# Optimization experiments

Measured on AMD Instinct MI355X. Metric: run time of the kernel, lower is better.

The kernel has to match this reference:

```python
import jax, jax.numpy as jnp
import numpy as np

B, S, D, R, H = 4, 2048, 1024, 256, 8
NI, NP, NO, K = 8, 32, 8, 3
DH = R // H


def _householder_chain(x, vs):
    # x: [B,S,R], vs: [B,S,K,R]; apply K Householder reflections sequentially
    def step(carry, v):
        vn = v * jax.lax.rsqrt(jnp.sum(v * v, axis=-1, keepdims=True) + 1e-8)
        vTx = jnp.sum(carry * vn, axis=-1, keepdims=True)
        return carry - 2.0 * vn * vTx, None
    out, _ = jax.lax.scan(step, x, jnp.moveaxis(vs, 2, 0))
    return out


def _circuit_down(x, in_neurons, proc_neurons, input_weights, proc_idx):
    # soft mixture of input-neuron projections: d_model -> rank
    all_proj = jnp.einsum('bsd,ndr->bsnr', x, in_neurons)
    xr = jnp.einsum('bsnr,bsn->bsr', all_proj, input_weights)
    return _householder_chain(xr, proc_neurons[proc_idx])


def setup_inputs():
    key = jax.random.key(0)
    ks = jax.random.split(key, 14)
    n = lambda k, shape, sc: jax.random.normal(k, shape, jnp.float32) * sc
    inv_d, inv_r = 1.0 / np.sqrt(D), 1.0 / np.sqrt(R)
    return {
        'x': n(ks[0], (B, S, D), 1.0),
        'q_in': n(ks[1], (NI, D, R), inv_d),
        'q_proc': n(ks[2], (NP, R), inv_r),
        'k_in': n(ks[3], (NI, D, R), inv_d),
        'k_proc': n(ks[4], (NP, R), inv_r),
        'v_in': n(ks[5], (NI, D, R), inv_d),
        'v_proc': n(ks[6], (NP, R), inv_r),
        'o_proc': n(ks[7], (NP, R), inv_r),
        'o_out': n(ks[8], (NO, R, D), inv_r),
        'rd_in': n(ks[9], (NI, D), inv_d),
        'rd_proc': n(ks[10], (NP, D), inv_d),
        'ru_out': n(ks[11], (NO, R), inv_r),
        'ru_proc': n(ks[12], (NP, R), inv_r),
    }


def reference(x, q_in, q_proc, k_in, k_proc, v_in, v_proc, o_proc, o_out,
              rd_in, rd_proc, ru_out, ru_proc):
    # --- router (down): soft input weights + top-k process indices ---
    input_weights = jax.nn.softmax(x @ rd_in.T, axis=-1)          # [B,S,NI]
    _, pidx = jax.lax.top_k(x @ rd_proc.T, K)                     # [B,S,K]

    q = _circuit_down(x, q_in, q_proc, input_weights, pidx)      # [B,S,R]
    k = _circuit_down(x, k_in, k_proc, input_weights, pidx)
    v = _circuit_down(x, v_in, v_proc, input_weights, pidx)

    qh = q.reshape(B, S, H, DH)
    kh = k.reshape(B, S, H, DH)
    vh = v.reshape(B, S, H, DH)
    scores = jnp.einsum('bqhd,bkhd->bhqk', qh, kh) / np.sqrt(DH)
    attn = jax.nn.softmax(scores, axis=-1)
    o = jnp.einsum('bhqk,bkhd->bqhd', attn, vh).reshape(B, S, R)  # [B,S,R]

    # --- router (up): soft output weights + top-k process indices ---
    output_weights = jax.nn.softmax(o @ ru_out.T, axis=-1)        # [B,S,NO]
    _, pidx_u = jax.lax.top_k(o @ ru_proc.T, K)                   # [B,S,K]

    oh = _householder_chain(o, o_proc[pidx_u])                    # [B,S,R]
    out = jnp.einsum('bsr,bsn,nrd->bsd', oh, output_weights, o_out)
    return out
```

## Files before the change

kernel.cpp:

```cpp
#include <hip/hip_runtime.h>
#include <math.h>

#define NI 8
#define NP 32
#define TOPK 3

typedef _Float16 f16;
typedef f16 f16x8 __attribute__((ext_vector_type(8)));
typedef f16 f16x4 __attribute__((ext_vector_type(4)));
typedef float f32x4 __attribute__((ext_vector_type(4)));

__device__ __forceinline__ float wave_sum(float v) {
  #pragma unroll
  for (int off = 32; off; off >>= 1) v += __shfl_xor(v, off);
  return v;
}

__device__ __forceinline__ void gload16(const void* g, void* l) {
  __builtin_amdgcn_global_load_lds(
      (const __attribute__((address_space(1))) unsigned int*)g,
      (__attribute__((address_space(3))) unsigned int*)l, 16, 0, 0);
}

__device__ __forceinline__ void split4(float4 v, f16x4& h, f16x4& l) {
  h[0] = (f16)v.x; l[0] = (f16)(v.x - (float)h[0]);
  h[1] = (f16)v.y; l[1] = (f16)(v.y - (float)h[1]);
  h[2] = (f16)v.z; l[2] = (f16)(v.z - (float)h[2]);
  h[3] = (f16)v.w; l[3] = (f16)(v.w - (float)h[3]);
}

template<int CHUNKS>
__global__ __launch_bounds__(256) void router_v2(
    const float* __restrict__ X,
    const float* __restrict__ Wsm,
    const float* __restrict__ Wtk,
    float* __restrict__ iw, int* __restrict__ pidx,
    f16* __restrict__ Xh, f16* __restrict__ Xl)
{
  const int Kin = CHUNKS * 256;
  const int tid = threadIdx.x, wave = tid >> 6, lane = tid & 63;
  __shared__ float sc[4][4][40];
  const size_t t0 = (size_t)blockIdx.x * 16 + wave * 4;

  float4 xv[4][CHUNKS];
  #pragma unroll
  for (int tt = 0; tt < 4; ++tt) {
    const float4* Xp = reinterpret_cast<const float4*>(X + (t0 + tt) * Kin);
    #pragma unroll
    for (int c = 0; c < CHUNKS; ++c) xv[tt][c] = Xp[c * 64 + lane];
  }
  if (Xh) {
    #pragma unroll
    for (int tt = 0; tt < 4; ++tt)
      #pragma unroll
      for (int c = 0; c < CHUNKS; ++c) {
        f16x4 h, l;
        split4(xv[tt][c], h, l);
        size_t off = (t0 + tt) * Kin + (c * 64 + lane) * 4;
        *reinterpret_cast<f16x4*>(Xh + off) = h;
        *reinterpret_cast<f16x4*>(Xl + off) = l;
      }
  }

  for (int w = 0; w < 40; ++w) {
    const float* Wr = (w < NI) ? (Wsm + (size_t)w * Kin) : (Wtk + (size_t)(w - NI) * Kin);
    const float4* Wp = reinterpret_cast<const float4*>(Wr);
    float p[4] = {};
    #pragma unroll
    for (int c = 0; c < CHUNKS; ++c) {
      float4 wv = Wp[c * 64 + lane];
      #pragma unroll
      for (int tt = 0; tt < 4; ++tt) {
        p[tt] = fmaf(xv[tt][c].x, wv.x, p[tt]);
        p[tt] = fmaf(xv[tt][c].y, wv.y, p[tt]);
        p[tt] = fmaf(xv[tt][c].z, wv.z, p[tt]);
        p[tt] = fmaf(xv[tt][c].w, wv.w, p[tt]);
      }
    }
    #pragma unroll
    for (int tt = 0; tt < 4; ++tt) {
      p[tt] = wave_sum(p[tt]);
      if (lane == 0) sc[wave][tt][w] = p[tt];
    }
  }

  for (int tt = 0; tt < 4; ++tt) {
    float s = (lane < NI) ? sc[wave][tt][lane] : -3.0e38f;
    float m = s;
    #pragma unroll
    for (int off = 4; off; off >>= 1) m = fmaxf(m, __shfl_xor(m, off));
    float e = expf(s - m);
    float sum = e;
    #pragma unroll
    for (int off = 4; off; off >>= 1) sum += __shfl_xor(sum, off);
    if (lane < NI) iw[(t0 + tt) * NI + lane] = e / sum;

    float v = (lane < NP) ? sc[wave][tt][NI + lane] : -3.0e38f;
    int idx = lane;
    #pragma unroll
    for (int j = 0; j < TOPK; ++j) {
      float bv = v; int bi = idx;
      #pragma unroll
      for (int off = 32; off; off >>= 1) {
        float ov = __shfl_xor(bv, off); int oi = __shfl_xor(bi, off);
        if (ov > bv || (ov == bv && oi < bi)) { bv = ov; bi = oi; }
      }
      if (lane == 0) pidx[(t0 + tt) * TOPK + j] = bi;
      if (idx == bi) v = -3.0e38f;
    }
  }
}

__global__ __launch_bounds__(256) void pack_bt(
    const float* __restrict__ S, f16* __restrict__ Dh, f16* __restrict__ Dl,
    int C, int K)
{
  __shared__ float T[64][65];
  const int tid = threadIdx.x;
  const int kb = blockIdx.x * 64, cb = blockIdx.y * 64;
  const int tr = tid >> 4, tc = (tid & 15) * 4;
  #pragma unroll
  for (int i = 0; i < 4; ++i) {
    float4 v = *reinterpret_cast<const float4*>(&S[(size_t)(kb + tr + i * 16) * C + cb + tc]);
    T[tr + i * 16][tc + 0] = v.x; T[tr + i * 16][tc + 1] = v.y;
    T[tr + i * 16][tc + 2] = v.z; T[tr + i * 16][tc + 3] = v.w;
  }
  __syncthreads();
  #pragma unroll
  for (int i = 0; i < 4; ++i) {
    int c = tr + i * 16;
    f16x4 vh, vl;
    #pragma unroll
    for (int q = 0; q < 4; ++q) {
      float a = T[tc + q][c];
      f16 h = (f16)a;
      vh[q] = h;
      vl[q] = (f16)(a - (float)h);
    }
    *reinterpret_cast<f16x4*>(&Dh[(size_t)(cb + c) * K + kb + tc]) = vh;
    *reinterpret_cast<f16x4*>(&Dl[(size_t)(cb + c) * K + kb + tc]) = vl;
  }
}

#define TBM 128
#define TBK 32

template<int NFRAG>
__global__ __launch_bounds__(256, 3) void gemm_split2(
    const f16* __restrict__ Xh, const f16* __restrict__ Xl, int Kin,
    const float* __restrict__ W,
    const f16* __restrict__ Bth, const f16* __restrict__ Btl,
    float* __restrict__ C, int ldC, int Ktot)
{
  const int TBN = 32 * NFRAG;
  __shared__ f16x8 AhL[512];
  __shared__ f16x8 AlL[512];
  __shared__ f16x8 BhL[TBN * 4];
  __shared__ f16x8 BlL[TBN * 4];
  __shared__ float Ws[TBM][NI];

  const int tid = threadIdx.x;
  const int wave = tid >> 6, lane = tid & 63;
  const int wm = wave >> 1, wn = wave & 1;
  const int fr = lane & 15, ks = lane >> 4;
  const int row0 = blockIdx.x * TBM, c0 = blockIdx.y * TBN;

  for (int i = tid; i < TBM * NI; i += 256)
    Ws[i >> 3][i & 7] = W[(size_t)(row0 + (i >> 3)) * NI + (i & 7)];

  const int s1 = 256 + tid;
  const int ar0 = tid >> 2, kg0 = ((tid & 3) - (ar0 >> 1)) & 3;
  const int ar1 = s1 >> 2,  kg1 = ((s1 & 3) - (ar1 >> 1)) & 3;

  const f16* xh0 = Xh + (size_t)(row0 + ar0) * Kin + kg0 * 8;
  const f16* xh1 = Xh + (size_t)(row0 + ar1) * Kin + kg1 * 8;
  const f16* xl0 = Xl + (size_t)(row0 + ar0) * Kin + kg0 * 8;
  const f16* xl1 = Xl + (size_t)(row0 + ar1) * Kin + kg1 * 8;
  const f16* bh0 = Bth + (size_t)(c0 + ar0) * Ktot + kg0 * 8;
  const f16* bl0 = Btl + (size_t)(c0 + ar0) * Ktot + kg0 * 8;
  const int ar1b = (ar1 < TBN) ? ar1 : 0;
  const f16* bh1 = Bth + (size_t)(c0 + ar1b) * Ktot + kg1 * 8;
  const f16* bl1 = Btl + (size_t)(c0 + ar1b) * Ktot + kg1 * 8;
  const bool b2 = (NFRAG == 4) || (wave < 2);

  f16x8* AhW = &AhL[wave * 64];
  f16x8* AlW = &AlL[wave * 64];
  f16x8* BhW = &BhL[wave * 64];
  f16x8* BlW = &BlL[wave * 64];

  f32x4 acc[4][NFRAG] = {};
  f32x4 cac[4][NFRAG] = {};

  int n = 0, dk0 = 0;
  for (int kt = 0; kt < Ktot; kt += TBK) {
    __syncthreads();
    gload16(xh0 + dk0, AhW);
    gload16(xh1 + dk0, AhW + 256);
    gload16(xl0 + dk0, AlW);
    gload16(xl1 + dk0, AlW + 256);
    gload16(bh0 + kt, BhW);
    gload16(bl0 + kt, BlW);
    if (b2) {
      gload16(bh1 + kt, BhW + 256);
      gload16(bl1 + kt, BlW + 256);
    }
    __syncthreads();

    f16x8 ah[4], al[4], bh[NFRAG], bl[NFRAG];
    #pragma unroll
    for (int mf = 0; mf < 4; ++mf) {
      int ar = wm * 64 + mf * 16 + fr;
      int sl = ar * 4 + (((ar >> 1) + ks) & 3);
      ah[mf] = AhL[sl]; al[mf] = AlL[sl];
    }
    #pragma unroll
    for (int nf = 0; nf < NFRAG; ++nf) {
      int bc = wn * (16 * NFRAG) + nf * 16 + fr;
      int sl = bc * 4 + (((bc >> 1) + ks) & 3);
      bh[nf] = BhL[sl]; bl[nf] = BlL[sl];
    }
    #pragma unroll
    for (int mf = 0; mf < 4; ++mf)
      #pragma unroll
      for (int nf = 0; nf < NFRAG; ++nf) {
        acc[mf][nf] = __builtin_amdgcn_mfma_f32_16x16x32_f16(ah[mf], bh[nf], acc[mf][nf], 0, 0, 0);
        acc[mf][nf] = __builtin_amdgcn_mfma_f32_16x16x32_f16(ah[mf], bl[nf], acc[mf][nf], 0, 0, 0);
        acc[mf][nf] = __builtin_amdgcn_mfma_f32_16x16x32_f16(al[mf], bh[nf], acc[mf][nf], 0, 0, 0);
      }

    dk0 += TBK;
    if (dk0 == Kin) {
      dk0 = 0;
      #pragma unroll
      for (int mf = 0; mf < 4; ++mf) {
        float w0 = Ws[wm * 64 + mf * 16 + ks * 4 + 0][n];
        float w1 = Ws[wm * 64 + mf * 16 + ks * 4 + 1][n];
        float w2 = Ws[wm * 64 + mf * 16 + ks * 4 + 2][n];
        float w3 = Ws[wm * 64 + mf * 16 + ks * 4 + 3][n];
        #pragma unroll
        for (int nf = 0; nf < NFRAG; ++nf) {
          cac[mf][nf][0] = fmaf(w0, acc[mf][nf][0], cac[mf][nf][0]);
          cac[mf][nf][1] = fmaf(w1, acc[mf][nf][1], cac[mf][nf][1]);
          cac[mf][nf][2] = fmaf(w2, acc[mf][nf][2], cac[mf][nf][2]);
          cac[mf][nf][3] = fmaf(w3, acc[mf][nf][3], cac[mf][nf][3]);
          acc[mf][nf] = (f32x4){0.f, 0.f, 0.f, 0.f};
        }
      }
      ++n;
    }
  }

  #pragma unroll
  for (int mf = 0; mf < 4; ++mf)
    #pragma unroll
    for (int nf = 0; nf < NFRAG; ++nf) {
      int col = c0 + wn * (16 * NFRAG) + nf * 16 + fr;
      #pragma unroll
      for (int j = 0; j < 4; ++j) {
        int row = row0 + wm * 64 + mf * 16 + ks * 4 + j;
        C[(size_t)row * ldC + col] = cac[mf][nf][j];
      }
    }
}

#define GBM 128
#define GBN 128
#define GBK 16
#define GBMp 132

__global__ __launch_bounds__(256) void gemm_mix(
    const float* __restrict__ X, int Kin,
    const float* __restrict__ W,
    const float* __restrict__ Bm0, const float* __restrict__ Bm1, const float* __restrict__ Bm2,
    int ldB, float* __restrict__ C, int ldC, int Nz)
{
  __shared__ float As[GBK][GBMp];
  __shared__ float Bs[GBK][GBMp];
  __shared__ float Ws[GBM][NI];
  const int tid = threadIdx.x;
  const int row0 = blockIdx.x * GBM;
  const int z = blockIdx.z;
  const float* Bm = (z == 0) ? Bm0 : (z == 1) ? Bm1 : Bm2;
  const int c0 = blockIdx.y * GBN;
  for (int i = tid; i < GBM * NI; i += 256)
    Ws[i >> 3][i & 7] = W[(size_t)(row0 + (i >> 3)) * NI + (i & 7)];
  __syncthreads();

  float acc[8][8] = {};
  const int tr = tid >> 4, tc = tid & 15;
  const int srow = tid >> 2;
  const int sseg = (tid & 3) * 4;
  const int bk = tid >> 4;
  const int bc = (tid & 15) * 4;

  const int Ktot = Kin * NI;
  int n = 0, dk0 = 0;
  for (int kt = 0; kt < Ktot; kt += GBK) {
    __syncthreads();
    #pragma unroll
    for (int p = 0; p < 2; ++p) {
      int r = p * 64 + srow;
      float4 xv = *reinterpret_cast<const float4*>(&X[(size_t)(row0 + r) * Kin + dk0 + sseg]);
      float wgt = Ws[r][n];
      As[sseg + 0][r] = xv.x * wgt;
      As[sseg + 1][r] = xv.y * wgt;
      As[sseg + 2][r] = xv.z * wgt;
      As[sseg + 3][r] = xv.w * wgt;
    }
    #pragma unroll
    for (int p = 0; p < 2; ++p) {
      int cc = p * 64 + bc;
      float4 bv = *reinterpret_cast<const float4*>(&Bm[(size_t)(kt + bk) * ldB + c0 + cc]);
      *reinterpret_cast<float4*>(&Bs[bk][cc]) = bv;
    }
    __syncthreads();
    #pragma unroll
    for (int k = 0; k < GBK; ++k) {
      float4 a0 = *reinterpret_cast<const float4*>(&As[k][tr * 8]);
      float4 a1 = *reinterpret_cast<const float4*>(&As[k][tr * 8 + 4]);
      float4 b0 = *reinterpret_cast<const float4*>(&Bs[k][tc * 8]);
      float4 b1 = *reinterpret_cast<const float4*>(&Bs[k][tc * 8 + 4]);
      float av[8] = {a0.x, a0.y, a0.z, a0.w, a1.x, a1.y, a1.z, a1.w};
      float bv[8] = {b0.x, b0.y, b0.z, b0.w, b1.x, b1.y, b1.z, b1.w};
      #pragma unroll
      for (int i = 0; i < 8; ++i)
        #pragma unroll
        for (int j = 0; j < 8; ++j)
          acc[i][j] = fmaf(av[i], bv[j], acc[i][j]);
    }
    dk0 += GBK;
    if (dk0 == Kin) { dk0 = 0; ++n; }
  }
  #pragma unroll
  for (int i = 0; i < 8; ++i) {
    int row = row0 + tr * 8 + i;
    float* Cp = C + (size_t)row * ldC + z * Nz + c0 + tc * 8;
    float4 o0 = {acc[i][0], acc[i][1], acc[i][2], acc[i][3]};
    float4 o1 = {acc[i][4], acc[i][5], acc[i][6], acc[i][7]};
    *reinterpret_cast<float4*>(Cp) = o0;
    *reinterpret_cast<float4*>(Cp + 4) = o1;
  }
}

__global__ __launch_bounds__(256) void hh_kernel(
    float* __restrict__ X, int ldX,
    const float* __restrict__ P0, const float* __restrict__ P1, const float* __restrict__ P2,
    const int* __restrict__ pidx,
    f16* __restrict__ D0h, f16* __restrict__ D0l,
    f16* __restrict__ D1h, f16* __restrict__ D1l,
    f16* __restrict__ D2h, f16* __restrict__ D2l)
{
  const int tid = threadIdx.x, wave = tid >> 6, lane = tid & 63;
  const int t = blockIdx.x * 4 + wave;
  const int circ = blockIdx.y;
  const float* P = (circ == 0) ? P0 : (circ == 1) ? P1 : P2;
  float* xp = X + (size_t)t * ldX + circ * 256;
  float4 x4 = *reinterpret_cast<float4*>(xp + lane * 4);
  #pragma unroll
  for (int j = 0; j < TOPK; ++j) {
    int id = pidx[t * TOPK + j];
    const float* vp = P + (size_t)id * 256;
    float4 v4 = *reinterpret_cast<const float4*>(vp + lane * 4);
    float ss = v4.x * v4.x + v4.y * v4.y + v4.z * v4.z + v4.w * v4.w;
    ss = wave_sum(ss);
    float inv = 1.0f / sqrtf(ss + 1e-8f);
    float4 vn = {v4.x * inv, v4.y * inv, v4.z * inv, v4.w * inv};
    float dt = vn.x * x4.x + vn.y * x4.y + vn.z * x4.z + vn.w * x4.w;
    dt = wave_sum(dt);
    float d2 = 2.0f * dt;
    x4.x = fmaf(-d2, vn.x, x4.x);
    x4.y = fmaf(-d2, vn.y, x4.y);
    x4.z = fmaf(-d2, vn.z, x4.z);
    x4.w = fmaf(-d2, vn.w, x4.w);
  }
  f16* Dh = (circ == 0) ? D0h : (circ == 1) ? D1h : D2h;
  f16* Dl = (circ == 0) ? D0l : (circ == 1) ? D1l : D2l;
  if (Dh) {
    f16x4 h, l;
    split4(x4, h, l);
    *reinterpret_cast<f16x4*>(Dh + (size_t)t * 256 + lane * 4) = h;
    *reinterpret_cast<f16x4*>(Dl + (size_t)t * 256 + lane * 4) = l;
  } else {
    *reinterpret_cast<float4*>(xp + lane * 4) = x4;
  }
}

__global__ __launch_bounds__(256, 2) void attn_mfma2(
    const float* __restrict__ qkv,
    const f16* __restrict__ Khg, const f16* __restrict__ Klg,
    const f16* __restrict__ Vhg, const f16* __restrict__ Vlg,
    float* __restrict__ O)
{
  __shared__ f16 Kh[64][40], Kl[64][40];
  __shared__ f16 Vh[32][72], Vl[32][72];
  __shared__ f16 Ph[4][32][72], Pl[4][32][72];

  const int tid = threadIdx.x, wave = tid >> 6, lane = tid & 63;
  const int c = lane & 15, g = lane >> 4;
  const int bh = blockIdx.y, b = bh >> 3, h = bh & 7;
  const int q0 = blockIdx.x * 128;
  const size_t tbase = (size_t)b * 2048;
  const float SCALE = 0.17677669529663687f;

  f16x8 qh[2], ql[2];
  #pragma unroll
  for (int qt = 0; qt < 2; ++qt) {
    const int row = q0 + wave * 32 + qt * 16 + c;
    const float* qp = qkv + (tbase + row) * 768 + h * 32 + g * 8;
    float4 a = *reinterpret_cast<const float4*>(qp);
    float4 b4 = *reinterpret_cast<const float4*>(qp + 4);
    float qv[8] = {a.x, a.y, a.z, a.w, b4.x, b4.y, b4.z, b4.w};
    #pragma unroll
    for (int j = 0; j < 8; ++j) {
      float xs = qv[j] * SCALE;
      f16 hh = (f16)xs;
      qh[qt][j] = hh;
      ql[qt][j] = (f16)(xs - (float)hh);
    }
  }

  f32x4 sacc[2][4];
  f32x4 oacc[2][2] = {};
  float mrow[2][4] = {{-INFINITY, -INFINITY, -INFINITY, -INFINITY},
                      {-INFINITY, -INFINITY, -INFINITY, -INFINITY}};
  float lrow[2][4] = {};

  for (int k0 = 0; k0 < 2048; k0 += 64) {
    __syncthreads();
    {
      const int kj = tid >> 2, dq = (tid & 3) * 8;
      const size_t krow = (tbase + k0 + kj) * 256 + h * 32 + dq;
      *reinterpret_cast<f16x8*>(&Kh[kj][dq]) = *reinterpret_cast<const f16x8*>(Khg + krow);
      *reinterpret_cast<f16x8*>(&Kl[kj][dq]) = *reinterpret_cast<const f16x8*>(Klg + krow);

      const int vk = tid & 63, vq = (tid >> 6) * 8;
      const size_t vrow = (tbase + k0 + vk) * 256 + h * 32 + vq;
      f16x8 vh8 = *reinterpret_cast<const f16x8*>(Vhg + vrow);
      f16x8 vl8 = *reinterpret_cast<const f16x8*>(Vlg + vrow);
      #pragma unroll
      for (int j = 0; j < 8; ++j) { Vh[vq + j][vk] = vh8[j]; Vl[vq + j][vk] = vl8[j]; }
    }
    __syncthreads();

    #pragma unroll
    for (int s = 0; s < 4; ++s) {
      f16x8 kbh = *reinterpret_cast<const f16x8*>(&Kh[s * 16 + c][g * 8]);
      f16x8 kbl = *reinterpret_cast<const f16x8*>(&Kl[s * 16 + c][g * 8]);
      #pragma unroll
      for (int qt = 0; qt < 2; ++qt) {
        f32x4 acc = {0.f, 0.f, 0.f, 0.f};
        acc = __builtin_amdgcn_mfma_f32_16x16x32_f16(qh[qt], kbh, acc, 0, 0, 0);
        acc = __builtin_amdgcn_mfma_f32_16x16x32_f16(qh[qt], kbl, acc, 0, 0, 0);
        acc = __builtin_amdgcn_mfma_f32_16x16x32_f16(ql[qt], kbh, acc, 0, 0, 0);
        sacc[qt][s] = acc;
      }
    }

    float alpha[2][4];
    #pragma unroll
    for (int qt = 0; qt < 2; ++qt)
      #pragma unroll
      for (int r = 0; r < 4; ++r) {
        float mt = fmaxf(fmaxf(sacc[qt][0][r], sacc[qt][1][r]),
                         fmaxf(sacc[qt][2][r], sacc[qt][3][r]));
        #pragma unroll
        for (int off = 1; off < 16; off <<= 1) mt = fmaxf(mt, __shfl_xor(mt, off));
        float mn = fmaxf(mrow[qt][r], mt);
        float al = __expf(mrow[qt][r] - mn);
        mrow[qt][r] = mn;
        alpha[qt][r] = al;
        float ps = 0.f;
        #pragma unroll
        for (int s = 0; s < 4; ++s) {
          float p = __expf(sacc[qt][s][r] - mn);
          sacc[qt][s][r] = p;
          ps += p;
        }
        #pragma unroll
        for (int off = 1; off < 16; off <<= 1) ps += __shfl_xor(ps, off);
        lrow[qt][r] = lrow[qt][r] * al + ps;
      }

    #pragma unroll
    for (int qt = 0; qt < 2; ++qt)
      #pragma unroll
      for (int s = 0; s < 4; ++s)
        #pragma unroll
        for (int r = 0; r < 4; ++r) {
          float p = sacc[qt][s][r];
          f16 hh = (f16)p;
          Ph[wave][qt * 16 + g * 4 + r][s * 16 + c] = hh;
          Pl[wave][qt * 16 + g * 4 + r][s * 16 + c] = (f16)(p - (float)hh);
        }

    #pragma unroll
    for (int qt = 0; qt < 2; ++qt)
      #pragma unroll
      for (int dh = 0; dh < 2; ++dh)
        #pragma unroll
        for (int r = 0; r < 4; ++r) oacc[qt][dh][r] *= alpha[qt][r];

    #pragma unroll
    for (int ch = 0; ch < 2; ++ch) {
      f16x8 pah[2], pal[2];
      #pragma unroll
      for (int qt = 0; qt < 2; ++qt) {
        pah[qt] = *reinterpret_cast<const f16x8*>(&Ph[wave][qt * 16 + c][ch * 32 + g * 8]);
        pal[qt] = *reinterpret_cast<const f16x8*>(&Pl[wave][qt * 16 + c][ch * 32 + g * 8]);
      }
      #pragma unroll
      for (int dh = 0; dh < 2; ++dh) {
        f16x8 vh = *reinterpret_cast<const f16x8*>(&Vh[dh * 16 + c][ch * 32 + g * 8]);
        f16x8 vl = *reinterpret_cast<const f16x8*>(&Vl[dh * 16 + c][ch * 32 + g * 8]);
        #pragma unroll
        for (int qt = 0; qt < 2; ++qt) {
          oacc[qt][dh] = __builtin_amdgcn_mfma_f32_16x16x32_f16(pah[qt], vh, oacc[qt][dh], 0, 0, 0);
          oacc[qt][dh] = __builtin_amdgcn_mfma_f32_16x16x32_f16(pah[qt], vl, oacc[qt][dh], 0, 0, 0);
          oacc[qt][dh] = __builtin_amdgcn_mfma_f32_16x16x32_f16(pal[qt], vh, oacc[qt][dh], 0, 0, 0);
        }
      }
    }
  }

  #pragma unroll
  for (int qt = 0; qt < 2; ++qt)
    #pragma unroll
    for (int r = 0; r < 4; ++r) {
      float inv = 1.0f / lrow[qt][r];
      int row = q0 + wave * 32 + qt * 16 + g * 4 + r;
      #pragma unroll
      for (int dh = 0; dh < 2; ++dh)
        O[(tbase + row) * 256 + h * 32 + dh * 16 + c] = oacc[qt][dh][r] * inv;
    }
}

__global__ __launch_bounds__(256) void attn_kernel(
    const float* __restrict__ qkv, float* __restrict__ O)
{
  const int tid = threadIdx.x;
  const int wave = tid >> 6, lane = tid & 63;
  const int bh = blockIdx.y, b = bh >> 3, h = bh & 7;
  const int q0 = blockIdx.x * 8;
  const size_t tbase = (size_t)b * 2048;
  const float SCALE = 0.17677669529663687f;

  __shared__ float Ks[64][36];
  __shared__ float Vt[32][68];
  __shared__ float Ps[4][2][64];

  const int wq = __builtin_amdgcn_readfirstlane(wave);
  const float* qr0 = qkv + (tbase + q0 + wq * 2) * 768 + h * 32;
  float qa[32], qb[32];
  #pragma unroll
  for (int i = 0; i < 32; ++i) { qa[i] = qr0[i]; qb[i] = qr0[768 + i]; }

  const int r = lane >> 5, d = lane & 31;
  float m0 = -INFINITY, m1 = -INFINITY, l0 = 0.f, l1 = 0.f, oacc = 0.f;

  for (int k0 = 0; k0 < 2048; k0 += 64) {
    __syncthreads();
    {
      int j = tid >> 2;
      int c = (tid & 3) * 8;
      const float* kp = qkv + (tbase + k0 + j) * 768 + 256 + h * 32 + c;
      float4 ka = *reinterpret_cast<const float4*>(kp);
      float4 kb = *reinterpret_cast<const float4*>(kp + 4);
      *reinterpret_cast<float4*>(&Ks[j][c]) = ka;
      *reinterpret_cast<float4*>(&Ks[j][c + 4]) = kb;
      const float* vp = qkv + (tbase + k0 + j) * 768 + 512 + h * 32 + c;
      float4 va = *reinterpret_cast<const float4*>(vp);
      float4 vb = *reinterpret_cast<const float4*>(vp + 4);
      Vt[c + 0][j] = va.x; Vt[c + 1][j] = va.y; Vt[c + 2][j] = va.z; Vt[c + 3][j] = va.w;
      Vt[c + 4][j] = vb.x; Vt[c + 5][j] = vb.y; Vt[c + 6][j] = vb.z; Vt[c + 7][j] = vb.w;
    }
    __syncthreads();
    float s0 = 0.f, s1 = 0.f;
    #pragma unroll
    for (int dd = 0; dd < 8; ++dd) {
      float4 kv = *reinterpret_cast<const float4*>(&Ks[lane][dd * 4]);
      s0 = fmaf(qa[dd * 4 + 0], kv.x, s0); s1 = fmaf(qb[dd * 4 + 0], kv.x, s1);
      s0 = fmaf(qa[dd * 4 + 1], kv.y, s0); s1 = fmaf(qb[dd * 4 + 1], kv.y, s1);
      s0 = fmaf(qa[dd * 4 + 2], kv.z, s0); s1 = fmaf(qb[dd * 4 + 2], kv.z, s1);
      s0 = fmaf(qa[dd * 4 + 3], kv.w, s0); s1 = fmaf(qb[dd * 4 + 3], kv.w, s1);
    }
    s0 *= SCALE; s1 *= SCALE;
    float mx0 = s0, mx1 = s1;
    #pragma unroll
    for (int off = 32; off; off >>= 1) {
      mx0 = fmaxf(mx0, __shfl_xor(mx0, off));
      mx1 = fmaxf(mx1, __shfl_xor(mx1, off));
    }
    float nm0 = fmaxf(m0, mx0), nm1 = fmaxf(m1, mx1);
    float p0 = expf(s0 - nm0), p1 = expf(s1 - nm1);
    float a0 = expf(m0 - nm0), a1 = expf(m1 - nm1);
    float sp0 = p0, sp1 = p1;
    #pragma unroll
    for (int off = 32; off; off >>= 1) {
      sp0 += __shfl_xor(sp0, off);
      sp1 += __shfl_xor(sp1, off);
    }
    l0 = l0 * a0 + sp0; l1 = l1 * a1 + sp1;
    m0 = nm0; m1 = nm1;
    Ps[wave][0][lane] = p0; Ps[wave][1][lane] = p1;
    oacc *= (r == 0) ? a0 : a1;
    #pragma unroll
    for (int jq = 0; jq < 16; ++jq) {
      float4 pv = *reinterpret_cast<const float4*>(&Ps[wave][r][jq * 4]);
      float4 vv = *reinterpret_cast<const float4*>(&Vt[d][jq * 4]);
      oacc = fmaf(pv.x, vv.x, oacc);
      oacc = fmaf(pv.y, vv.y, oacc);
      oacc = fmaf(pv.z, vv.z, oacc);
      oacc = fmaf(pv.w, vv.w, oacc);
    }
  }
  float lf = (r == 0) ? l0 : l1;
  oacc /= lf;
  O[(tbase + q0 + wave * 2 + r) * 256 + h * 32 + d] = oacc;
}

extern "C" void kernel_launch(void* const* d_in, const int* in_sizes, int n_in,
                              void* d_out, int out_size, void* d_ws, size_t ws_size,
                              hipStream_t stream) {
  const float* x       = (const float*)d_in[0];
  const float* q_in    = (const float*)d_in[1];
  const float* q_proc  = (const float*)d_in[2];
  const float* k_in    = (const float*)d_in[3];
  const float* k_proc  = (const float*)d_in[4];
  const float* v_in    = (const float*)d_in[5];
  const float* v_proc  = (const float*)d_in[6];
  const float* o_proc  = (const float*)d_in[7];
  const float* o_out   = (const float*)d_in[8];
  const float* rd_in   = (const float*)d_in[9];
  const float* rd_proc = (const float*)d_in[10];
  const float* ru_out  = (const float*)d_in[11];
  const float* ru_proc = (const float*)d_in[12];
  float* out = (float*)d_out;
  float* qkv = (float*)d_out;

  const size_t NEED2 = (768ull << 10) + 768ull * 8192 * 2 * 2 + 8192ull * 1024 * 2 * 2;

  if (ws_size >= NEED2) {
    char* wsb = (char*)d_ws;
    float* iw    = (float*)wsb;
    float* owt   = (float*)(wsb + (256 << 10));
    int*   pidx  = (int*)(wsb + (512 << 10));
    int*   pidxu = (int*)(wsb + (640 << 10));
    char*  R1    = wsb + (768 << 10);
    f16* bth_q = (f16*)R1;
    f16* btl_q = (f16*)(R1 + 768ull * 8192 * 2);
    char*  R2    = R1 + 768ull * 8192 * 2 * 2;
    f16* Xh = (f16*)R2;
    f16* Xl = (f16*)(R2 + 8192ull * 1024 * 2);
    float* obuf  = (float*)R2;
    f16* Oh    = (f16*)(R2 + 8388608);
    f16* Ol    = (f16*)(R2 + 12582912);
    f16* bth_o = (f16*)(R2 + 16777216);
    f16* btl_o = (f16*)(R2 + 20971520);
    f16* Khg   = (f16*)(R2 + 25165824);
    f16* Klg   = (f16*)(R2 + 29360128);
    f16* Vhg = (f16*)((char*)d_out + 25165824);
    f16* Vlg = (f16*)((char*)d_out + 29360128);

    router_v2<4><<<dim3(512), dim3(256), 0, stream>>>(x, rd_in, rd_proc, iw, pidx, Xh, Xl);
    pack_bt<<<dim3(128, 4), dim3(256), 0, stream>>>(q_in, bth_q,                 btl_q,                 256, 8192);
    pack_bt<<<dim3(128, 4), dim3(256), 0, stream>>>(k_in, bth_q + 256ull * 8192, btl_q + 256ull * 8192, 256, 8192);
    pack_bt<<<dim3(128, 4), dim3(256), 0, stream>>>(v_in, bth_q + 512ull * 8192, btl_q + 512ull * 8192, 256, 8192);
    gemm_split2<3><<<dim3(64, 8), dim3(256), 0, stream>>>(Xh, Xl, 1024, iw, bth_q, btl_q,
                                                          qkv, 768, 8192);
    hh_kernel<<<dim3(2048, 3), dim3(256), 0, stream>>>(qkv, 768, q_proc, k_proc, v_proc, pidx,
                                                       (f16*)nullptr, (f16*)nullptr,
                                                       Khg, Klg, Vhg, Vlg);
    pack_bt<<<dim3(32, 16), dim3(256), 0, stream>>>(o_out, bth_o, btl_o, 1024, 2048);
    attn_mfma2<<<dim3(16, 32), dim3(256), 0, stream>>>(qkv, Khg, Klg, Vhg, Vlg, obuf);
    router_v2<1><<<dim3(512), dim3(256), 0, stream>>>(obuf, ru_out, ru_proc, owt, pidxu,
                                                      (f16*)nullptr, (f16*)nullptr);
    hh_kernel<<<dim3(2048, 1), dim3(256), 0, stream>>>(obuf, 256, o_proc, o_proc, o_proc, pidxu,
                                                       Oh, Ol,
                                                       (f16*)nullptr, (f16*)nullptr,
                                                       (f16*)nullptr, (f16*)nullptr);
    gemm_split2<4><<<dim3(64, 8), dim3(256), 0, stream>>>(Oh, Ol, 256, owt, bth_o, btl_o,
                                                          out, 1024, 2048);
  } else {
    float* ws = (float*)d_ws;
    float* iw    = ws;
    int*   pidx  = (int*)(ws + 65536);
    float* obuf  = ws + 65536 + 24576;
    float* owt   = obuf + 8192 * 256;
    int*   pidxu = (int*)(owt + 65536);

    router_v2<4><<<dim3(512), dim3(256), 0, stream>>>(x, rd_in, rd_proc, iw, pidx,
                                                      (f16*)nullptr, (f16*)nullptr);
    gemm_mix<<<dim3(64, 2, 3), dim3(256), 0, stream>>>(x, 1024, iw, q_in, k_in, v_in,
                                                       256, qkv, 768, 256);
    hh_kernel<<<dim3(2048, 3), dim3(256), 0, stream>>>(qkv, 768, q_proc, k_proc, v_proc, pidx,
                                                       (f16*)nullptr, (f16*)nullptr,
                                                       (f16*)nullptr, (f16*)nullptr,
                                                       (f16*)nullptr, (f16*)nullptr);
    attn_kernel<<<dim3(256, 32), dim3(256), 0, stream>>>(qkv, obuf);
    router_v2<1><<<dim3(512), dim3(256), 0, stream>>>(obuf, ru_out, ru_proc, owt, pidxu,
                                                      (f16*)nullptr, (f16*)nullptr);
    hh_kernel<<<dim3(2048, 1), dim3(256), 0, stream>>>(obuf, 256, o_proc, o_proc, o_proc, pidxu,
                                                       (f16*)nullptr, (f16*)nullptr,
                                                       (f16*)nullptr, (f16*)nullptr,
                                                       (f16*)nullptr, (f16*)nullptr);
    gemm_mix<<<dim3(64, 8, 1), dim3(256), 0, stream>>>(obuf, 256, owt, o_out, o_out, o_out,
                                                       1024, out, 1024, 1024);
  }
}
```

Measured before the change: 743.5 us.

## Double-buffer QKV GEMM LDS tiles and register-prefetch attention K/V blocks

Adds a double-buffered variant of the split-f16 QKV projection GEMM. It issues async global-to-LDS loads for the next K tile before computing the current one, with explicit vmcnt waits and barriers. The attention kernel now prefetches the next K/V block into registers while computing the current block, so global load latency overlaps MFMA work. The cost is doubled LDS use in the GEMM, with launch bounds dropping to 2 blocks per SM, and extra registers held live in attention.

```diff
diff --git a/kernel.cpp b/kernel.cpp
--- a/kernel.cpp
+++ b/kernel.cpp
@@ -142,8 +142,138 @@
   }
 }
 
+#define TBK 32
+
+__global__ __launch_bounds__(256, 2) void gemm_split2db(
+    const f16* __restrict__ Xh, const f16* __restrict__ Xl, int Kin,
+    const float* __restrict__ W,
+    const f16* __restrict__ Bth, const f16* __restrict__ Btl,
+    float* __restrict__ C, int ldC, int Ktot)
+{
+  __shared__ f16x8 AhL[2][512];
+  __shared__ f16x8 AlL[2][512];
+  __shared__ f16x8 BhL[2][384];
+  __shared__ f16x8 BlL[2][384];
+  __shared__ float Ws[128][NI];
+
+  const int tid = threadIdx.x;
+  const int wave = tid >> 6, lane = tid & 63;
+  const int wm = wave >> 1, wn = wave & 1;
+  const int fr = lane & 15, ks = lane >> 4;
+  const int row0 = blockIdx.x * 128, c0 = blockIdx.y * 96;
+
+  for (int i = tid; i < 128 * NI; i += 256)
+    Ws[i >> 3][i & 7] = W[(size_t)(row0 + (i >> 3)) * NI + (i & 7)];
+  __syncthreads();
+
+  const int s1a = 256 + tid;
+  const int ar0 = tid >> 2,  kg0 = ((tid & 3) - (ar0 >> 1)) & 3;
+  const int ar1 = s1a >> 2,  kg1 = ((s1a & 3) - (ar1 >> 1)) & 3;
+  const int s1b = 256 + (tid & 127);
+  const int br1 = s1b >> 2,  kgb = ((s1b & 3) - (br1 >> 1)) & 3;
+
+  const f16* xh0 = Xh + (size_t)(row0 + ar0) * Kin + kg0 * 8;
+  const f16* xh1 = Xh + (size_t)(row0 + ar1) * Kin + kg1 * 8;
+  const f16* xl0 = Xl + (size_t)(row0 + ar0) * Kin + kg0 * 8;
+  const f16* xl1 = Xl + (size_t)(row0 + ar1) * Kin + kg1 * 8;
+  const f16* bh0 = Bth + (size_t)(c0 + ar0) * Ktot + kg0 * 8;
+  const f16* bl0 = Btl + (size_t)(c0 + ar0) * Ktot + kg0 * 8;
+  const f16* bh1 = Bth + (size_t)(c0 + br1) * Ktot + kgb * 8;
+  const f16* bl1 = Btl + (size_t)(c0 + br1) * Ktot + kgb * 8;
+
+  auto STAGE = [&](int buf, int dkx, int ktb) {
+    f16x8* Ah = &AhL[buf][wave * 64];
+    f16x8* Al = &AlL[buf][wave * 64];
+    f16x8* Bh = &BhL[buf][wave * 64];
+    f16x8* Bl = &BlL[buf][wave * 64];
+    f16x8* Bh1 = &BhL[buf][256 + (wave & 1) * 64];
+    f16x8* Bl1 = &BlL[buf][256 + (wave & 1) * 64];
+    gload16(xh0 + dkx, Ah);
+    gload16(xh1 + dkx, Ah + 256);
+    gload16(xl0 + dkx, Al);
+    gload16(xl1 + dkx, Al + 256);
+    gload16(bh0 + ktb, Bh);
+    gload16(bh1 + ktb, Bh1);
+    gload16(bl0 + ktb, Bl);
+    gload16(bl1 + ktb, Bl1);
+  };
+
+  f32x4 acc[4][3] = {};
+  f32x4 cac[4][3] = {};
+
+  STAGE(0, 0, 0);
+  int n = 0, dk0 = 0;
+  for (int kt = 0; kt < Ktot; kt += TBK) {
+    const int cur = (kt >> 5) & 1;
+    int dkn = dk0 + TBK; if (dkn == Kin) dkn = 0;
+    if (kt + TBK < Ktot) {
+      STAGE(cur ^ 1, dkn, kt + TBK);
+      asm volatile("s_waitcnt vmcnt(8)" ::: "memory");
+    } else {
+      asm volatile("s_waitcnt vmcnt(0)" ::: "memory");
+    }
+    __builtin_amdgcn_s_barrier();
+    __builtin_amdgcn_sched_barrier(0);
+
+    f16x8 ah[4], al[4], bh[3], bl[3];
+    #pragma unroll
+    for (int mf = 0; mf < 4; ++mf) {
+      int ar = wm * 64 + mf * 16 + fr;
+      int sl = ar * 4 + (((ar >> 1) + ks) & 3);
+      ah[mf] = AhL[cur][sl]; al[mf] = AlL[cur][sl];
+    }
+    #pragma unroll
+    for (int nf = 0; nf < 3; ++nf) {
+      int bc = wn * 48 + nf * 16 + fr;
+      int sl = bc * 4 + (((bc >> 1) + ks) & 3);
+      bh[nf] = BhL[cur][sl]; bl[nf] = BlL[cur][sl];
+    }
+    #pragma unroll
+    for (int mf = 0; mf < 4; ++mf)
+      #pragma unroll
+      for (int nf = 0; nf < 3; ++nf) {
+        acc[mf][nf] = __builtin_amdgcn_mfma_f32_16x16x32_f16(ah[mf], bh[nf], acc[mf][nf], 0, 0, 0);
+        acc[mf][nf] = __builtin_amdgcn_mfma_f32_16x16x32_f16(ah[mf], bl[nf], acc[mf][nf], 0, 0, 0);
+        acc[mf][nf] = __builtin_amdgcn_mfma_f32_16x16x32_f16(al[mf], bh[nf], acc[mf][nf], 0, 0, 0);
+      }
+
+    if (dkn == 0) {
+      #pragma unroll
+      for (int mf = 0; mf < 4; ++mf) {
+        float w0 = Ws[wm * 64 + mf * 16 + ks * 4 + 0][n];
+        float w1 = Ws[wm * 64 + mf * 16 + ks * 4 + 1][n];
+        float w2 = Ws[wm * 64 + mf * 16 + ks * 4 + 2][n];
+        float w3 = Ws[wm * 64 + mf * 16 + ks * 4 + 3][n];
+        #pragma unroll
+        for (int nf = 0; nf < 3; ++nf) {
+          cac[mf][nf][0] = fmaf(w0, acc[mf][nf][0], cac[mf][nf][0]);
+          cac[mf][nf][1] = fmaf(w1, acc[mf][nf][1], cac[mf][nf][1]);
+          cac[mf][nf][2] = fmaf(w2, acc[mf][nf][2], cac[mf][nf][2]);
+          cac[mf][nf][3] = fmaf(w3, acc[mf][nf][3], cac[mf][nf][3]);
+          acc[mf][nf] = (f32x4){0.f, 0.f, 0.f, 0.f};
+        }
+      }
+      ++n;
+    }
+    dk0 = dkn;
+    __builtin_amdgcn_s_barrier();
+    __builtin_amdgcn_sched_barrier(0);
+  }
+
+  #pragma unroll
+  for (int mf = 0; mf < 4; ++mf)
+    #pragma unroll
+    for (int nf = 0; nf < 3; ++nf) {
+      int col = c0 + wn * 48 + nf * 16 + fr;
+      #pragma unroll
+      for (int j = 0; j < 4; ++j) {
+        int row = row0 + wm * 64 + mf * 16 + ks * 4 + j;
+        C[(size_t)row * ldC + col] = cac[mf][nf][j];
+      }
+    }
+}
+
 #define TBM 128
-#define TBK 32
 
 template<int NFRAG>
 __global__ __launch_bounds__(256, 3) void gemm_split2(
@@ -419,6 +549,19 @@
     }
   }
 
+  const int kj = tid >> 2, dq = (tid & 3) * 8;
+  const int vk = tid & 63, vq = (tid >> 6) * 8;
+
+  f16x8 rkh, rkl, rvh, rvl;
+  {
+    const size_t krow = (tbase + kj) * 256 + h * 32 + dq;
+    rkh = *reinterpret_cast<const f16x8*>(Khg + krow);
+    rkl = *reinterpret_cast<const f16x8*>(Klg + krow);
+    const size_t vrow = (tbase + vk) * 256 + h * 32 + vq;
+    rvh = *reinterpret_cast<const f16x8*>(Vhg + vrow);
+    rvl = *reinterpret_cast<const f16x8*>(Vlg + vrow);
+  }
+
   f32x4 sacc[2][4];
   f32x4 oacc[2][2] = {};
   float mrow[2][4] = {{-INFINITY, -INFINITY, -INFINITY, -INFINITY},
@@ -428,19 +571,20 @@
   for (int k0 = 0; k0 < 2048; k0 += 64) {
     __syncthreads();
     {
-      const int kj = tid >> 2, dq = (tid & 3) * 8;
-      const size_t krow = (tbase + k0 + kj) * 256 + h * 32 + dq;
-      *reinterpret_cast<f16x8*>(&Kh[kj][dq]) = *reinterpret_cast<const f16x8*>(Khg + krow);
-      *reinterpret_cast<f16x8*>(&Kl[kj][dq]) = *reinterpret_cast<const f16x8*>(Klg + krow);
-
-      const int vk = tid & 63, vq = (tid >> 6) * 8;
-      const size_t vrow = (tbase + k0 + vk) * 256 + h * 32 + vq;
-      f16x8 vh8 = *reinterpret_cast<const f16x8*>(Vhg + vrow);
-      f16x8 vl8 = *reinterpret_cast<const f16x8*>(Vlg + vrow);
-      #pragma unroll
-      for (int j = 0; j < 8; ++j) { Vh[vq + j][vk] = vh8[j]; Vl[vq + j][vk] = vl8[j]; }
+      *reinterpret_cast<f16x8*>(&Kh[kj][dq]) = rkh;
+      *reinterpret_cast<f16x8*>(&Kl[kj][dq]) = rkl;
+      #pragma unroll
+      for (int j = 0; j < 8; ++j) { Vh[vq + j][vk] = rvh[j]; Vl[vq + j][vk] = rvl[j]; }
     }
     __syncthreads();
+    if (k0 + 64 < 2048) {
+      const size_t krow = (tbase + k0 + 64 + kj) * 256 + h * 32 + dq;
+      rkh = *reinterpret_cast<const f16x8*>(Khg + krow);
+      rkl = *reinterpret_cast<const f16x8*>(Klg + krow);
+      const size_t vrow = (tbase + k0 + 64 + vk) * 256 + h * 32 + vq;
+      rvh = *reinterpret_cast<const f16x8*>(Vhg + vrow);
+      rvl = *reinterpret_cast<const f16x8*>(Vlg + vrow);
+    }
 
     #pragma unroll
     for (int s = 0; s < 4; ++s) {
@@ -665,8 +809,8 @@
     pack_bt<<<dim3(128, 4), dim3(256), 0, stream>>>(q_in, bth_q,                 btl_q,                 256, 8192);
     pack_bt<<<dim3(128, 4), dim3(256), 0, stream>>>(k_in, bth_q + 256ull * 8192, btl_q + 256ull * 8192, 256, 8192);
     pack_bt<<<dim3(128, 4), dim3(256), 0, stream>>>(v_in, bth_q + 512ull * 8192, btl_q + 512ull * 8192, 256, 8192);
-    gemm_split2<3><<<dim3(64, 8), dim3(256), 0, stream>>>(Xh, Xl, 1024, iw, bth_q, btl_q,
-                                                          qkv, 768, 8192);
+    gemm_split2db<<<dim3(64, 8), dim3(256), 0, stream>>>(Xh, Xl, 1024, iw, bth_q, btl_q,
+                                                         qkv, 768, 8192);
     hh_kernel<<<dim3(2048, 3), dim3(256), 0, stream>>>(qkv, 768, q_proc, k_proc, v_proc, pidx,
                                                        (f16*)nullptr, (f16*)nullptr,
                                                        Khg, Klg, Vhg, Vlg);
```

Result: no change. 745.8 us (+0.3%).

## Fuse K/V hi-lo split into attention and prefetch next K/V tile

Applied to the files above, without the earlier changes.

The attention kernel now reads fp32 K and V straight from the qkv buffer and does the f16 hi/lo split itself, so the Householder kernel no longer writes separate hi/lo K/V arrays. The next 64-row K/V tile is prefetched into registers while the current tile is processed. V and P are kept in LDS as packed hi/lo 32-bit words and unpacked on read. In exchange, every query block redoes the split conversion and pays extra ALU work for packing and unpacking, and register pressure rises.

```diff
diff --git a/kernel.cpp b/kernel.cpp
--- a/kernel.cpp
+++ b/kernel.cpp
@@ -27,6 +27,28 @@
   h[1] = (f16)v.y; l[1] = (f16)(v.y - (float)h[1]);
   h[2] = (f16)v.z; l[2] = (f16)(v.z - (float)h[2]);
   h[3] = (f16)v.w; l[3] = (f16)(v.w - (float)h[3]);
+}
+
+__device__ __forceinline__ unsigned int pack_f16x2(float x) {
+  f16 h = (f16)x;
+  f16 l = (f16)(x - (float)h);
+  return (unsigned int)__builtin_bit_cast(unsigned short, h)
+       | ((unsigned int)__builtin_bit_cast(unsigned short, l) << 16);
+}
+
+__device__ __forceinline__ void unpack8(const unsigned int* p, f16x8& hi, f16x8& lo) {
+  uint4 w0 = *reinterpret_cast<const uint4*>(p);
+  uint4 w1 = *reinterpret_cast<const uint4*>(p + 4);
+  union { unsigned int u[4]; f16x8 v; } H, L;
+  H.u[0] = (w0.x & 0xffffu) | (w0.y << 16);
+  L.u[0] = (w0.x >> 16)     | (w0.y & 0xffff0000u);
+  H.u[1] = (w0.z & 0xffffu) | (w0.w << 16);
+  L.u[1] = (w0.z >> 16)     | (w0.w & 0xffff0000u);
+  H.u[2] = (w1.x & 0xffffu) | (w1.y << 16);
+  L.u[2] = (w1.x >> 16)     | (w1.y & 0xffff0000u);
+  H.u[3] = (w1.z & 0xffffu) | (w1.w << 16);
+  L.u[3] = (w1.z >> 16)     | (w1.w & 0xffff0000u);
+  hi = H.v; lo = L.v;
 }
 
 template<int CHUNKS>
@@ -385,15 +407,13 @@
   }
 }
 
-__global__ __launch_bounds__(256, 2) void attn_mfma2(
-    const float* __restrict__ qkv,
-    const f16* __restrict__ Khg, const f16* __restrict__ Klg,
-    const f16* __restrict__ Vhg, const f16* __restrict__ Vlg,
-    float* __restrict__ O)
+__global__ __launch_bounds__(256, 2) void attn_mfma(
+    const float* __restrict__ qkv, float* __restrict__ O)
 {
-  __shared__ f16 Kh[64][40], Kl[64][40];
-  __shared__ f16 Vh[32][72], Vl[32][72];
-  __shared__ f16 Ph[4][32][72], Pl[4][32][72];
+  __shared__ f16 Kh[64][40];
+  __shared__ f16 Kl[64][40];
+  __shared__ unsigned int Vtp[32][68];
+  __shared__ unsigned int Pp[4][32][68];
 
   const int tid = threadIdx.x, wave = tid >> 6, lane = tid & 63;
   const int c = lane & 15, g = lane >> 4;
@@ -419,6 +439,19 @@
     }
   }
 
+  const int kj = tid >> 2, dq = (tid & 3) * 8;
+  const int vk = tid & 63, vq = (tid >> 6) * 8;
+
+  float4 rka, rkb, rva, rvb;
+  {
+    const float* kp = qkv + (tbase + kj) * 768 + 256 + h * 32 + dq;
+    rka = *reinterpret_cast<const float4*>(kp);
+    rkb = *reinterpret_cast<const float4*>(kp + 4);
+    const float* vp = qkv + (tbase + vk) * 768 + 512 + h * 32 + vq;
+    rva = *reinterpret_cast<const float4*>(vp);
+    rvb = *reinterpret_cast<const float4*>(vp + 4);
+  }
+
   f32x4 sacc[2][4];
   f32x4 oacc[2][2] = {};
   float mrow[2][4] = {{-INFINITY, -INFINITY, -INFINITY, -INFINITY},
@@ -428,19 +461,30 @@
   for (int k0 = 0; k0 < 2048; k0 += 64) {
     __syncthreads();
     {
-      const int kj = tid >> 2, dq = (tid & 3) * 8;
-      const size_t krow = (tbase + k0 + kj) * 256 + h * 32 + dq;
-      *reinterpret_cast<f16x8*>(&Kh[kj][dq]) = *reinterpret_cast<const f16x8*>(Khg + krow);
-      *reinterpret_cast<f16x8*>(&Kl[kj][dq]) = *reinterpret_cast<const f16x8*>(Klg + krow);
-
-      const int vk = tid & 63, vq = (tid >> 6) * 8;
-      const size_t vrow = (tbase + k0 + vk) * 256 + h * 32 + vq;
-      f16x8 vh8 = *reinterpret_cast<const f16x8*>(Vhg + vrow);
-      f16x8 vl8 = *reinterpret_cast<const f16x8*>(Vlg + vrow);
-      #pragma unroll
-      for (int j = 0; j < 8; ++j) { Vh[vq + j][vk] = vh8[j]; Vl[vq + j][vk] = vl8[j]; }
+      float kv[8] = {rka.x, rka.y, rka.z, rka.w, rkb.x, rkb.y, rkb.z, rkb.w};
+      f16x8 khi, klo;
+      #pragma unroll
+      for (int j = 0; j < 8; ++j) {
+        f16 hh = (f16)kv[j];
+        khi[j] = hh;
+        klo[j] = (f16)(kv[j] - (float)hh);
+      }
+      *reinterpret_cast<f16x8*>(&Kh[kj][dq]) = khi;
+      *reinterpret_cast<f16x8*>(&Kl[kj][dq]) = klo;
+
+      float vv[8] = {rva.x, rva.y, rva.z, rva.w, rvb.x, rvb.y, rvb.z, rvb.w};
+      #pragma unroll
+      for (int j = 0; j < 8; ++j) Vtp[vq + j][vk] = pack_f16x2(vv[j]);
     }
     __syncthreads();
+    if (k0 + 64 < 2048) {
+      const float* kp = qkv + (tbase + k0 + 64 + kj) * 768 + 256 + h * 32 + dq;
+      rka = *reinterpret_cast<const float4*>(kp);
+      rkb = *reinterpret_cast<const float4*>(kp + 4);
+      const float* vp = qkv + (tbase + k0 + 64 + vk) * 768 + 512 + h * 32 + vq;
+      rva = *reinterpret_cast<const float4*>(vp);
+      rvb = *reinterpret_cast<const float4*>(vp + 4);
+    }
 
     #pragma unroll
     for (int s = 0; s < 4; ++s) {
@@ -486,12 +530,8 @@
       #pragma unroll
       for (int s = 0; s < 4; ++s)
         #pragma unroll
-        for (int r = 0; r < 4; ++r) {
-          float p = sacc[qt][s][r];
-          f16 hh = (f16)p;
-          Ph[wave][qt * 16 + g * 4 + r][s * 16 + c] = hh;
-          Pl[wave][qt * 16 + g * 4 + r][s * 16 + c] = (f16)(p - (float)hh);
-        }
+        for (int r = 0; r < 4; ++r)
+          Pp[wave][qt * 16 + g * 4 + r][s * 16 + c] = pack_f16x2(sacc[qt][s][r]);
 
     #pragma unroll
     for (int qt = 0; qt < 2; ++qt)
@@ -504,14 +544,12 @@
     for (int ch = 0; ch < 2; ++ch) {
       f16x8 pah[2], pal[2];
       #pragma unroll
-      for (int qt = 0; qt < 2; ++qt) {
-        pah[qt] = *reinterpret_cast<const f16x8*>(&Ph[wave][qt * 16 + c][ch * 32 + g * 8]);
-        pal[qt] = *reinterpret_cast<const f16x8*>(&Pl[wave][qt * 16 + c][ch * 32 + g * 8]);
-      }
+      for (int qt = 0; qt < 2; ++qt)
+        unpack8(&Pp[wave][qt * 16 + c][ch * 32 + g * 8], pah[qt], pal[qt]);
       #pragma unroll
       for (int dh = 0; dh < 2; ++dh) {
-        f16x8 vh = *reinterpret_cast<const f16x8*>(&Vh[dh * 16 + c][ch * 32 + g * 8]);
-        f16x8 vl = *reinterpret_cast<const f16x8*>(&Vl[dh * 16 + c][ch * 32 + g * 8]);
+        f16x8 vh, vl;
+        unpack8(&Vtp[dh * 16 + c][ch * 32 + g * 8], vh, vl);
         #pragma unroll
         for (int qt = 0; qt < 2; ++qt) {
           oacc[qt][dh] = __builtin_amdgcn_mfma_f32_16x16x32_f16(pah[qt], vh, oacc[qt][dh], 0, 0, 0);
@@ -656,10 +694,6 @@
     f16* Ol    = (f16*)(R2 + 12582912);
     f16* bth_o = (f16*)(R2 + 16777216);
     f16* btl_o = (f16*)(R2 + 20971520);
-    f16* Khg   = (f16*)(R2 + 25165824);
-    f16* Klg   = (f16*)(R2 + 29360128);
-    f16* Vhg = (f16*)((char*)d_out + 25165824);
-    f16* Vlg = (f16*)((char*)d_out + 29360128);
 
     router_v2<4><<<dim3(512), dim3(256), 0, stream>>>(x, rd_in, rd_proc, iw, pidx, Xh, Xl);
     pack_bt<<<dim3(128, 4), dim3(256), 0, stream>>>(q_in, bth_q,                 btl_q,                 256, 8192);
@@ -669,9 +703,10 @@
                                                           qkv, 768, 8192);
     hh_kernel<<<dim3(2048, 3), dim3(256), 0, stream>>>(qkv, 768, q_proc, k_proc, v_proc, pidx,
                                                        (f16*)nullptr, (f16*)nullptr,
-                                                       Khg, Klg, Vhg, Vlg);
+                                                       (f16*)nullptr, (f16*)nullptr,
+                                                       (f16*)nullptr, (f16*)nullptr);
     pack_bt<<<dim3(32, 16), dim3(256), 0, stream>>>(o_out, bth_o, btl_o, 1024, 2048);
-    attn_mfma2<<<dim3(16, 32), dim3(256), 0, stream>>>(qkv, Khg, Klg, Vhg, Vlg, obuf);
+    attn_mfma<<<dim3(16, 32), dim3(256), 0, stream>>>(qkv, obuf);
     router_v2<1><<<dim3(512), dim3(256), 0, stream>>>(obuf, ru_out, ru_proc, owt, pidxu,
                                                       (f16*)nullptr, (f16*)nullptr);
     hh_kernel<<<dim3(2048, 1), dim3(256), 0, stream>>>(obuf, 256, o_proc, o_proc, o_proc, pidxu,
```

After: 728.9 us. 2.0% less time.
